# Kernel optimization log

Hardware: AMD Instinct MI355X
Metric: run time of the kernel (lower is better)

## Reference

```python
import math
import jax, jax.numpy as jnp
import numpy as np

N_HEADS = 16
D_EMBED = 1024
D_HEAD = D_EMBED // N_HEADS


def setup_inputs() -> dict:
    key = jax.random.key(0)
    k1, k2, k3, k4, k5 = jax.random.split(key, 5)
    B, S, D = 4, 2048, D_EMBED
    scale = 1.0 / math.sqrt(D)
    return {
        "x": jax.random.normal(k1, (B, S, D), dtype=jnp.float32),
        "in_proj_w": jax.random.normal(k2, (3 * D, D), dtype=jnp.float32) * scale,
        "in_proj_b": jax.random.normal(k3, (3 * D,), dtype=jnp.float32) * 0.02,
        "out_proj_w": jax.random.normal(k4, (D, D), dtype=jnp.float32) * scale,
        "out_proj_b": jax.random.normal(k5, (D,), dtype=jnp.float32) * 0.02,
        "causal_mask": 0,
    }


def reference(x, in_proj_w, in_proj_b, out_proj_w, out_proj_b, causal_mask):
    B, S, D = x.shape
    # in_proj: torch Linear -> x @ W^T + b, then chunk into q,k,v
    qkv = x @ in_proj_w.T + in_proj_b              # [B,S,3D]
    q, k, v = jnp.split(qkv, 3, axis=-1)
    # [B,S,D] -> [B,H,S,d]
    def heads(t):
        return t.reshape(B, S, N_HEADS, D_HEAD).transpose(0, 2, 1, 3)
    q, k, v = heads(q), heads(k), heads(v)
    weight = jnp.einsum("bhsd,bhtd->bhst", q, k)   # [B,H,S,S] materialized scores
    if causal_mask:
        mask = jnp.triu(jnp.ones((S, S), dtype=bool), k=1)
        weight = jnp.where(mask, -jnp.inf, weight)
    weight = jax.nn.softmax(weight / math.sqrt(D_HEAD), axis=-1)
    out = jnp.einsum("bhst,bhtd->bhsd", weight, v)  # [B,H,S,d]
    out = out.transpose(0, 2, 1, 3).reshape(B, S, D)
    return out @ out_proj_w.T + out_proj_b
```

## Files before the change

### kernel.cpp

```cpp
#include <hip/hip_runtime.h>

typedef unsigned short u16;
typedef _Float16 h8 __attribute__((ext_vector_type(8)));
typedef __fp16 fp16x2 __attribute__((ext_vector_type(2)));
typedef float f32x4 __attribute__((ext_vector_type(4)));

constexpr int B_ = 4, S_ = 2048, D_ = 1024, H_ = 16;

__device__ __forceinline__ void async16(const void* g, void* l) {
  __builtin_amdgcn_global_load_lds(
      (const __attribute__((address_space(1))) void*)g,
      (__attribute__((address_space(3))) void*)l, 16, 0, 0);
}

__device__ __forceinline__ unsigned pk2(float a, float b) {
  union { fp16x2 h; unsigned u; } c;
  c.h = __builtin_amdgcn_cvt_pkrtz(a, b);
  return c.u;
}

__global__ __launch_bounds__(256) void cvt_kernel(
    const float* __restrict__ src, _Float16* __restrict__ dst, int n)
{
  const int i = (blockIdx.x * 256 + threadIdx.x) * 4;
  if (i >= n) return;
  const float4 v = *(const float4*)(src + i);
  uint2 o;
  o.x = pk2(v.x, v.y);
  o.y = pk2(v.z, v.w);
  *(uint2*)(dst + i) = o;
}

template<bool OUT_HALF>
__global__ __launch_bounds__(256) void gemm_f16(
    const _Float16* __restrict__ A, const _Float16* __restrict__ Bw,
    const float* __restrict__ bias, void* __restrict__ Cout,
    int M, int N, int K)
{
  __shared__ __align__(16) _Float16 sA[4096];
  __shared__ __align__(16) _Float16 sB[4096];

  const int tid = threadIdx.x;
  const int lane = tid & 63, w = tid >> 6;
  const int wm = w & 1, wn = w >> 1;
  const int m0 = blockIdx.y * 128, n0 = blockIdx.x * 128;

  const int sr = 16 * w + (lane & 15);
  const int ss = lane >> 4;
  const _Float16* gA1 = A + (size_t)(m0 + sr) * K + 8 * ss;
  const _Float16* gA2 = gA1 + (size_t)64 * K;
  const _Float16* gB1 = Bw + (size_t)(n0 + sr) * K + 8 * ss;
  const _Float16* gB2 = gB1 + (size_t)64 * K;
  _Float16* lA1 = &sA[w * 512];
  _Float16* lA2 = &sA[(w + 4) * 512];
  _Float16* lB1 = &sB[w * 512];
  _Float16* lB2 = &sB[(w + 4) * 512];

  const f32x4 zf = {0.f, 0.f, 0.f, 0.f};
  f32x4 acc[4][4];
#pragma unroll
  for (int i = 0; i < 4; ++i)
#pragma unroll
    for (int j = 0; j < 4; ++j) acc[i][j] = zf;

  for (int k0 = 0; k0 < K; k0 += 32) {
    __syncthreads();
    async16(gA1 + k0, lA1);
    async16(gA2 + k0, lA2);
    async16(gB1 + k0, lB1);
    async16(gB2 + k0, lB2);
    __syncthreads();

    h8 fa[4], fb[4];
#pragma unroll
    for (int i = 0; i < 4; ++i) {
      fa[i] = *(const h8*)&sA[((wm * 4 + i) << 9) + (lane << 3)];
      fb[i] = *(const h8*)&sB[((wn * 4 + i) << 9) + (lane << 3)];
    }
#pragma unroll
    for (int i = 0; i < 4; ++i)
#pragma unroll
      for (int j = 0; j < 4; ++j)
        acc[i][j] = __builtin_amdgcn_mfma_f32_16x16x32_f16(fa[i], fb[j], acc[i][j], 0, 0, 0);
  }

  const int g = lane >> 4, cc = lane & 15;
#pragma unroll
  for (int j = 0; j < 4; ++j) {
    const int col = n0 + (wn * 4 + j) * 16 + cc;
    const float bv = bias[col];
#pragma unroll
    for (int i = 0; i < 4; ++i) {
      const int rowb = m0 + (wm * 4 + i) * 16 + g * 4;
#pragma unroll
      for (int r = 0; r < 4; ++r) {
        const float v = acc[i][j][r] + bv;
        if constexpr (OUT_HALF)
          ((_Float16*)Cout)[(size_t)(rowb + r) * N + col] = (_Float16)v;
        else
          ((float*)Cout)[(size_t)(rowb + r) * N + col] = v;
      }
    }
  }
}

__global__ __launch_bounds__(256) void transpose_v(
    const u16* __restrict__ qkv, u16* __restrict__ vT)
{
  __shared__ u16 T[64 * 73];
  const int tid = threadIdx.x;
  const int bh = blockIdx.y, s0 = blockIdx.x * 64;
  const int b = bh >> 4, h = bh & 15;
#pragma unroll
  for (int t = 0; t < 2; ++t) {
    const int c = tid + t * 256, r = c >> 3, cs = c & 7;
    union { int4 v; u16 s[8]; } u;
    u.v = *(const int4*)(qkv + (size_t)(b * S_ + s0 + r) * 3072 + 2048 + h * 64 + 8 * cs);
#pragma unroll
    for (int i = 0; i < 8; ++i) T[r * 73 + 8 * cs + i] = u.s[i];
  }
  __syncthreads();
#pragma unroll
  for (int t = 0; t < 2; ++t) {
    const int c = tid + t * 256, rd = c >> 3, ss = c & 7;
    union { int4 v; u16 s[8]; } u;
#pragma unroll
    for (int i = 0; i < 8; ++i) u.s[i] = T[(8 * ss + i) * 73 + rd];
    *(int4*)(vT + (size_t)(bh * 64 + rd) * S_ + s0 + 8 * ss) = u.v;
  }
}

__global__ __launch_bounds__(256, 4) void attn_f16(
    const _Float16* __restrict__ qkv, const _Float16* __restrict__ vT,
    _Float16* __restrict__ attnO, const int* __restrict__ causal_ptr)
{
  __shared__ __align__(16) _Float16 sQP[9216];
  __shared__ __align__(16) _Float16 sK[4096];
  __shared__ __align__(16) _Float16 sV[4096];

  const int tid = threadIdx.x, lane = tid & 63, w = tid >> 6;
  const int q4 = lane >> 4, cc = lane & 15;
  const int bh = blockIdx.y, b = bh >> 4, h = bh & 15;
  const int q0 = blockIdx.x * 128;
  const int causal = causal_ptr[0];

  {
    const int rr = lane & 15, sc8 = lane >> 4;
#pragma unroll
    for (int tt = 0; tt < 2; ++tt) {
      const int t = 2 * w + tt;
#pragma unroll
      for (int sh = 0; sh < 2; ++sh) {
        const _Float16* g = qkv + (size_t)(b * S_ + q0 + 16 * t + rr) * 3072 + h * 64 + 8 * (4 * sh + sc8);
        async16(g, &sQP[t * 1024 + sh * 512]);
      }
    }
  }
  __syncthreads();

  h8 qf[2][2];
#pragma unroll
  for (int m = 0; m < 2; ++m)
#pragma unroll
    for (int kk = 0; kk < 2; ++kk) {
      h8 v = *(const h8*)&sQP[((2 * w + m) << 10) + (kk << 9) + (lane << 3)];
      qf[m][kk] = v * (_Float16)0.125f;
    }

  h8 ones;
#pragma unroll
  for (int i = 0; i < 8; ++i) ones[i] = (_Float16)1.0f;

  const _Float16* gK = qkv + (size_t)(b * S_ + 16 * w + (lane & 15)) * 3072 + 1024 + h * 64 + 8 * (lane >> 4);
  const _Float16* gV = vT + (size_t)(bh * 64 + 16 * w + (lane & 15)) * S_ + 8 * (lane >> 4);
  _Float16* lK0 = &sK[w * 1024];
  _Float16* lV0 = &sV[w * 1024];

  const int wp = w * 2304;

  const f32x4 zf = {0.f, 0.f, 0.f, 0.f};
  f32x4 oa[2][4], lac[2];
#pragma unroll
  for (int m = 0; m < 2; ++m) {
    lac[m] = zf;
#pragma unroll
    for (int nt = 0; nt < 4; ++nt) oa[m][nt] = zf;
  }

  for (int j0 = 0; j0 < S_; j0 += 64) {
    if (causal && j0 > q0 + 127) break;
    __syncthreads();
    async16(gK + (size_t)j0 * 3072, lK0);
    async16(gK + (size_t)j0 * 3072 + 32, lK0 + 512);
    async16(gV + j0, lV0);
    async16(gV + j0 + 32, lV0 + 512);
    __syncthreads();

    f32x4 sc[2][4];
#pragma unroll
    for (int nt = 0; nt < 4; ++nt) {
      const h8 kf0 = *(const h8*)&sK[(nt << 10) + (lane << 3)];
      const h8 kf1 = *(const h8*)&sK[(nt << 10) + 512 + (lane << 3)];
#pragma unroll
      for (int m = 0; m < 2; ++m) {
        sc[m][nt] = __builtin_amdgcn_mfma_f32_16x16x32_f16(kf0, qf[m][0], zf, 0, 0, 0);
        sc[m][nt] = __builtin_amdgcn_mfma_f32_16x16x32_f16(kf1, qf[m][1], sc[m][nt], 0, 0, 0);
      }
    }

    if (causal) {
#pragma unroll
      for (int m = 0; m < 2; ++m)
#pragma unroll
        for (int nt = 0; nt < 4; ++nt)
#pragma unroll
          for (int r = 0; r < 4; ++r)
            if ((j0 + nt * 16 + q4 * 4 + r) > (q0 + 32 * w + m * 16 + cc))
              sc[m][nt][r] = -1.0e30f;
    }

#pragma unroll
    for (int m = 0; m < 2; ++m)
#pragma unroll
      for (int nt = 0; nt < 4; ++nt) {
        uint2 pk;
        pk.x = pk2(__expf(sc[m][nt][0]), __expf(sc[m][nt][1]));
        pk.y = pk2(__expf(sc[m][nt][2]), __expf(sc[m][nt][3]));
        *(uint2*)&sQP[wp + (m * 16 + cc) * 72 + nt * 16 + q4 * 4] = pk;
      }

    asm volatile("s_waitcnt lgkmcnt(0)" ::: "memory");

    h8 pf[2][2];
#pragma unroll
    for (int m = 0; m < 2; ++m)
#pragma unroll
      for (int kk = 0; kk < 2; ++kk)
        pf[m][kk] = *(const h8*)&sQP[wp + (m * 16 + cc) * 72 + kk * 32 + q4 * 8];

#pragma unroll
    for (int m = 0; m < 2; ++m) {
      lac[m] = __builtin_amdgcn_mfma_f32_16x16x32_f16(pf[m][0], ones, lac[m], 0, 0, 0);
      lac[m] = __builtin_amdgcn_mfma_f32_16x16x32_f16(pf[m][1], ones, lac[m], 0, 0, 0);
    }
#pragma unroll
    for (int nt = 0; nt < 4; ++nt) {
      const h8 vf0 = *(const h8*)&sV[(nt << 10) + (lane << 3)];
      const h8 vf1 = *(const h8*)&sV[(nt << 10) + 512 + (lane << 3)];
#pragma unroll
      for (int m = 0; m < 2; ++m) {
        oa[m][nt] = __builtin_amdgcn_mfma_f32_16x16x32_f16(pf[m][0], vf0, oa[m][nt], 0, 0, 0);
        oa[m][nt] = __builtin_amdgcn_mfma_f32_16x16x32_f16(pf[m][1], vf1, oa[m][nt], 0, 0, 0);
      }
    }
  }

#pragma unroll
  for (int m = 0; m < 2; ++m) {
    float inv[4];
#pragma unroll
    for (int r = 0; r < 4; ++r) inv[r] = 1.0f / lac[m][r];
#pragma unroll
    for (int nt = 0; nt < 4; ++nt) {
      const int col = h * 64 + nt * 16 + cc;
#pragma unroll
      for (int r = 0; r < 4; ++r) {
        const int row = b * S_ + q0 + 32 * w + m * 16 + q4 * 4 + r;
        attnO[(size_t)row * D_ + col] = (_Float16)(oa[m][nt][r] * inv[r]);
      }
    }
  }
}

extern "C" void kernel_launch(void* const* d_in, const int* in_sizes, int n_in,
                              void* d_out, int out_size, void* d_ws, size_t ws_size,
                              hipStream_t stream)
{
  const float* x  = (const float*)d_in[0];
  const float* wi = (const float*)d_in[1];
  const float* bi = (const float*)d_in[2];
  const float* wo = (const float*)d_in[3];
  const float* bo = (const float*)d_in[4];
  const int* causal = (const int*)d_in[5];

  _Float16* xh   = (_Float16*)d_ws;
  _Float16* wih  = xh + 8388608;
  _Float16* woh  = wih + 3145728;
  _Float16* qkvb = woh + 1048576;
  _Float16* vT   = qkvb + 25165824;
  _Float16* attn = vT + 8388608;

  const int M = B_ * S_;

  cvt_kernel<<<8192, 256, 0, stream>>>(x, xh, M * D_);
  cvt_kernel<<<3072, 256, 0, stream>>>(wi, wih, 3 * D_ * D_);
  cvt_kernel<<<1024, 256, 0, stream>>>(wo, woh, D_ * D_);

  gemm_f16<true><<<dim3(24, 64), 256, 0, stream>>>(
      xh, wih, bi, qkvb, M, 3 * D_, D_);

  transpose_v<<<dim3(32, 64), 256, 0, stream>>>((const u16*)qkvb, (u16*)vT);

  attn_f16<<<dim3(16, 64), 256, 0, stream>>>(qkvb, vT, attn, causal);

  gemm_f16<false><<<dim3(8, 64), 256, 0, stream>>>(
      attn, woh, bo, d_out, M, D_, D_);
}
```

Before: 325.9 us.

## Double-buffer LDS tiles in GEMM and attention loops to prefetch next tile

Both the f16 GEMM and the attention kernel now use two LDS buffers for their streamed tiles (A/B in the GEMM, K/V in attention). The first tile is loaded before the loop, and each iteration issues async loads for the next tile before computing on the current one, dropping one barrier per iteration. This is meant to hide global-to-LDS latency behind MFMA work. In exchange it doubles the K/V LDS footprint in attention, which may cut resident blocks per CU below the declared occupancy of 4.

```diff
diff --git a/kernel.cpp b/kernel.cpp
--- a/kernel.cpp
+++ b/kernel.cpp
@@ -37,8 +37,8 @@
     const float* __restrict__ bias, void* __restrict__ Cout,
     int M, int N, int K)
 {
-  __shared__ __align__(16) _Float16 sA[4096];
-  __shared__ __align__(16) _Float16 sB[4096];
+  __shared__ __align__(16) _Float16 sA[2][4096];
+  __shared__ __align__(16) _Float16 sB[2][4096];
 
   const int tid = threadIdx.x;
   const int lane = tid & 63, w = tid >> 6;
@@ -51,10 +51,6 @@
   const _Float16* gA2 = gA1 + (size_t)64 * K;
   const _Float16* gB1 = Bw + (size_t)(n0 + sr) * K + 8 * ss;
   const _Float16* gB2 = gB1 + (size_t)64 * K;
-  _Float16* lA1 = &sA[w * 512];
-  _Float16* lA2 = &sA[(w + 4) * 512];
-  _Float16* lB1 = &sB[w * 512];
-  _Float16* lB2 = &sB[(w + 4) * 512];
 
   const f32x4 zf = {0.f, 0.f, 0.f, 0.f};
   f32x4 acc[4][4];
@@ -63,19 +59,28 @@
 #pragma unroll
     for (int j = 0; j < 4; ++j) acc[i][j] = zf;
 
-  for (int k0 = 0; k0 < K; k0 += 32) {
+  async16(gA1, &sA[0][w * 512]);
+  async16(gA2, &sA[0][(w + 4) * 512]);
+  async16(gB1, &sB[0][w * 512]);
+  async16(gB2, &sB[0][(w + 4) * 512]);
+
+  const int NIT = K >> 5;
+  for (int it = 0; it < NIT; ++it) {
+    const int cur = it & 1;
     __syncthreads();
-    async16(gA1 + k0, lA1);
-    async16(gA2 + k0, lA2);
-    async16(gB1 + k0, lB1);
-    async16(gB2 + k0, lB2);
-    __syncthreads();
+    if (it + 1 < NIT) {
+      const int kn = (it + 1) << 5;
+      async16(gA1 + kn, &sA[cur ^ 1][w * 512]);
+      async16(gA2 + kn, &sA[cur ^ 1][(w + 4) * 512]);
+      async16(gB1 + kn, &sB[cur ^ 1][w * 512]);
+      async16(gB2 + kn, &sB[cur ^ 1][(w + 4) * 512]);
+    }
 
     h8 fa[4], fb[4];
 #pragma unroll
     for (int i = 0; i < 4; ++i) {
-      fa[i] = *(const h8*)&sA[((wm * 4 + i) << 9) + (lane << 3)];
-      fb[i] = *(const h8*)&sB[((wn * 4 + i) << 9) + (lane << 3)];
+      fa[i] = *(const h8*)&sA[cur][((wm * 4 + i) << 9) + (lane << 3)];
+      fb[i] = *(const h8*)&sB[cur][((wn * 4 + i) << 9) + (lane << 3)];
     }
 #pragma unroll
     for (int i = 0; i < 4; ++i)
@@ -135,8 +140,8 @@
     _Float16* __restrict__ attnO, const int* __restrict__ causal_ptr)
 {
   __shared__ __align__(16) _Float16 sQP[9216];
-  __shared__ __align__(16) _Float16 sK[4096];
-  __shared__ __align__(16) _Float16 sV[4096];
+  __shared__ __align__(16) _Float16 sK[2][4096];
+  __shared__ __align__(16) _Float16 sV[2][4096];
 
   const int tid = threadIdx.x, lane = tid & 63, w = tid >> 6;
   const int q4 = lane >> 4, cc = lane & 15;
@@ -156,6 +161,15 @@
       }
     }
   }
+
+  const _Float16* gK = qkv + (size_t)(b * S_ + 16 * w + (lane & 15)) * 3072 + 1024 + h * 64 + 8 * (lane >> 4);
+  const _Float16* gV = vT + (size_t)(bh * 64 + 16 * w + (lane & 15)) * S_ + 8 * (lane >> 4);
+
+  async16(gK, &sK[0][w * 1024]);
+  async16(gK + 32, &sK[0][w * 1024 + 512]);
+  async16(gV, &sV[0][w * 1024]);
+  async16(gV + 32, &sV[0][w * 1024 + 512]);
+
   __syncthreads();
 
   h8 qf[2][2];
@@ -171,11 +185,6 @@
 #pragma unroll
   for (int i = 0; i < 8; ++i) ones[i] = (_Float16)1.0f;
 
-  const _Float16* gK = qkv + (size_t)(b * S_ + 16 * w + (lane & 15)) * 3072 + 1024 + h * 64 + 8 * (lane >> 4);
-  const _Float16* gV = vT + (size_t)(bh * 64 + 16 * w + (lane & 15)) * S_ + 8 * (lane >> 4);
-  _Float16* lK0 = &sK[w * 1024];
-  _Float16* lV0 = &sV[w * 1024];
-
   const int wp = w * 2304;
 
   const f32x4 zf = {0.f, 0.f, 0.f, 0.f};
@@ -187,20 +196,25 @@
     for (int nt = 0; nt < 4; ++nt) oa[m][nt] = zf;
   }
 
-  for (int j0 = 0; j0 < S_; j0 += 64) {
-    if (causal && j0 > q0 + 127) break;
+  const int nit = causal ? (q0 / 64 + 2) : (S_ / 64);
+
+  for (int it = 0; it < nit; ++it) {
+    const int cur = it & 1;
+    const int j0 = it * 64;
     __syncthreads();
-    async16(gK + (size_t)j0 * 3072, lK0);
-    async16(gK + (size_t)j0 * 3072 + 32, lK0 + 512);
-    async16(gV + j0, lV0);
-    async16(gV + j0 + 32, lV0 + 512);
-    __syncthreads();
+    if (it + 1 < nit) {
+      const size_t jn = (size_t)(j0 + 64);
+      async16(gK + jn * 3072, &sK[cur ^ 1][w * 1024]);
+      async16(gK + jn * 3072 + 32, &sK[cur ^ 1][w * 1024 + 512]);
+      async16(gV + jn, &sV[cur ^ 1][w * 1024]);
+      async16(gV + jn + 32, &sV[cur ^ 1][w * 1024 + 512]);
+    }
 
     f32x4 sc[2][4];
 #pragma unroll
     for (int nt = 0; nt < 4; ++nt) {
-      const h8 kf0 = *(const h8*)&sK[(nt << 10) + (lane << 3)];
-      const h8 kf1 = *(const h8*)&sK[(nt << 10) + 512 + (lane << 3)];
+      const h8 kf0 = *(const h8*)&sK[cur][(nt << 10) + (lane << 3)];
+      const h8 kf1 = *(const h8*)&sK[cur][(nt << 10) + 512 + (lane << 3)];
 #pragma unroll
       for (int m = 0; m < 2; ++m) {
         sc[m][nt] = __builtin_amdgcn_mfma_f32_16x16x32_f16(kf0, qf[m][0], zf, 0, 0, 0);
@@ -245,8 +259,8 @@
     }
 #pragma unroll
     for (int nt = 0; nt < 4; ++nt) {
-      const h8 vf0 = *(const h8*)&sV[(nt << 10) + (lane << 3)];
-      const h8 vf1 = *(const h8*)&sV[(nt << 10) + 512 + (lane << 3)];
+      const h8 vf0 = *(const h8*)&sV[cur][(nt << 10) + (lane << 3)];
+      const h8 vf1 = *(const h8*)&sV[cur][(nt << 10) + 512 + (lane << 3)];
 #pragma unroll
       for (int m = 0; m < 2; ++m) {
         oa[m][nt] = __builtin_amdgcn_mfma_f32_16x16x32_f16(pf[m][0], vf0, oa[m][nt], 0, 0, 0);
```

New measurement: 363.1 us. +11.4%, slower.
